# Optimization experiments

Measured on AMD Instinct MI355X. Metric: run time of the kernel, lower is better.

Reference implementation:

```python
import jax, jax.numpy as jnp
import numpy as np

B = 4194304
RAD2DEG = 180.0 / np.pi


def setup_inputs() -> dict:
    key = jax.random.key(0)
    k1, k2, k3 = jax.random.split(key, 3)
    label = jax.random.normal(k1, (B, 3, 2), dtype=jnp.float32)
    est_label = jax.random.normal(k2, (B, 6), dtype=jnp.float32)
    mix_way = jax.random.randint(k3, (B,), 0, 2, dtype=jnp.int32)  # 0='single', 1=mixed
    return {"label": label, "est_label": est_label, "mix_way": mix_way}


def reference(label, est_label, mix_way):
    # --- permutation-invariant MSE loss ---
    e1, e2 = est_label[:, :3], est_label[:, 3:]            # [B,3] each
    l1, l2 = label[:, :, 0], label[:, :, 1]                 # [B,3] each
    mse = lambda a, b: jnp.mean((a - b) ** 2, axis=-1)      # per-batch mean over 3 comps
    loss_perm1 = mse(e1, l1) + mse(e2, l2)                  # [B]
    loss_perm2 = mse(e2, l1) + mse(e1, l2)                  # [B]
    mixed_loss = jnp.minimum(loss_perm1, loss_perm2)        # [B]
    # 'single' branch in the original uses the FULL (unindexed) tensors -> same scalar each time
    single_loss = jnp.mean((est_label[:, :3] - label[:, :, 0]) ** 2)
    per_batch = jnp.where(mix_way == 0, single_loss, mixed_loss)
    label_loss = jnp.mean(per_batch)

    # --- azimuth MAE with angle wrap-around and best pairing ---
    lab_az1 = jnp.arctan2(label[:, 1, 0], label[:, 0, 0]) * RAD2DEG
    lab_az2 = jnp.arctan2(label[:, 1, 1], label[:, 0, 1]) * RAD2DEG
    est_az1 = jnp.arctan2(est_label[:, 1], est_label[:, 0]) * RAD2DEG
    est_az2 = jnp.arctan2(est_label[:, 4], est_label[:, 3]) * RAD2DEG

    def wrap(e):
        e = jnp.abs(e)
        return jnp.where(e > 180.0, 360.0 - e, e)

    e11 = wrap(lab_az1 - est_az1)
    e22 = wrap(lab_az2 - est_az2)
    e12 = wrap(lab_az1 - est_az2)
    e21 = wrap(lab_az2 - est_az1)

    use_direct = (e11 + e22) < (e12 + e21)
    mae1 = jnp.mean(jnp.where(use_direct, e11, e12))
    mae2 = jnp.mean(jnp.where(use_direct, e22, e21))

    return (label_loss, mae1, mae2)
```

## Files before the change

### kernel.cpp

```cpp
#include <hip/hip_runtime.h>
#include <math.h>

#define RAD2DEG 57.29577951308232f

constexpr int S1_BLOCKS = 2048;
constexpr int S1_TPB    = 256;
constexpr int CHUNK     = 256;
constexpr int CH_F      = CHUNK * 12;
constexpr int CH_V4     = CHUNK * 3;

typedef __attribute__((address_space(1))) const unsigned int gu32;
typedef __attribute__((address_space(3))) unsigned int       lu32;

__device__ __forceinline__ void g2lds16(const float4* g, float* lds) {
    __builtin_amdgcn_global_load_lds((gu32*)g, (lu32*)lds, 16, 0, 0);
}

__device__ __forceinline__ float angdist_deg(float ax, float ay,
                                             float bx, float by) {
    float dot = ax * bx + ay * by;
    float cr  = fabsf(ay * bx - ax * by);
    float ad  = fabsf(dot);
    float mn  = fminf(cr, ad);
    float mx  = fmaxf(cr, ad);
    float t   = mn * __builtin_amdgcn_rcpf(fmaxf(mx, 1e-37f));
    float s   = t * t;
    float p = fmaf(s, -0.01172120f, 0.05265332f);
    p = fmaf(s, p, -0.11643287f);
    p = fmaf(s, p,  0.19354346f);
    p = fmaf(s, p, -0.33262347f);
    p = fmaf(s, p,  0.99997726f);
    float a = t * p;
    a = (cr > ad)    ? (1.57079632679489662f - a) : a;
    a = (dot < 0.0f) ? (3.14159265358979323f - a) : a;
    return a * RAD2DEG;
}

__device__ __forceinline__ void per_row(
    float l1x, float l2x, float l1y, float l2y, float l1z, float l2z,
    float e1x, float e1y, float e1z, float e2x, float e2y, float e2z,
    int mw,
    float& sS, float& sM, float& sC0, float& sM1, float& sM2)
{
    float dx, dy, dz;
    dx = e1x - l1x; dy = e1y - l1y; dz = e1z - l1z;
    float d11 = dx*dx + dy*dy + dz*dz;
    dx = e2x - l2x; dy = e2y - l2y; dz = e2z - l2z;
    float d22 = dx*dx + dy*dy + dz*dz;
    dx = e2x - l1x; dy = e2y - l1y; dz = e2z - l1z;
    float d21 = dx*dx + dy*dy + dz*dz;
    dx = e1x - l2x; dy = e1y - l2y; dz = e1z - l2z;
    float d12 = dx*dx + dy*dy + dz*dz;

    sS += d11;

    float mixed = fminf(d11 + d22, d21 + d12) * (1.0f / 3.0f);
    float m = (mw != 0) ? 1.0f : 0.0f;
    sM  += m * mixed;
    sC0 += 1.0f - m;

    float e11 = angdist_deg(l1x, l1y, e1x, e1y);
    float e22 = angdist_deg(l2x, l2y, e2x, e2y);
    float e12 = angdist_deg(l1x, l1y, e2x, e2y);
    float e21 = angdist_deg(l2x, l2y, e1x, e1y);

    bool ud = (e11 + e22) < (e12 + e21);
    sM1 += ud ? e11 : e12;
    sM2 += ud ? e22 : e21;
}

__global__ __launch_bounds__(S1_TPB) void stage1_kernel(
    const float* __restrict__ label,
    const float* __restrict__ est,
    const int*   __restrict__ mix,
    float* __restrict__ partials,
    int P)
{
    __shared__ float labS[CH_F];
    __shared__ float estS[CH_F];

    const int tid  = threadIdx.x;
    const int wid  = tid >> 6;
    const int lane = tid & 63;

    const float4* lab4 = (const float4*)label;
    const float4* est4 = (const float4*)est;
    const int2*   mix2 = (const int2*)mix;

    float sS = 0.f, sM = 0.f, sC0 = 0.f, sM1 = 0.f, sM2 = 0.f;

    const int nchunks = P / CHUNK;
    for (int c = blockIdx.x; c < nchunks; c += gridDim.x) {
        const int vbase = c * CH_V4;
        #pragma unroll
        for (int j = 0; j < 3; ++j) {
            const int vi = j * 256 + wid * 64;
            g2lds16(lab4 + vbase + vi + lane, labS + vi * 4);
            g2lds16(est4 + vbase + vi + lane, estS + vi * 4);
        }
        int2 mw = mix2[c * CHUNK + tid];
        __syncthreads();

        const float4* Lv = (const float4*)(labS + tid * 12);
        const float4* Ev = (const float4*)(estS + tid * 12);
        float4 L0 = Lv[0], L1 = Lv[1], L2 = Lv[2];
        float4 E0 = Ev[0], E1 = Ev[1], E2 = Ev[2];

        per_row(L0.x, L0.y, L0.z, L0.w, L1.x, L1.y,
                E0.x, E0.y, E0.z, E0.w, E1.x, E1.y,
                mw.x, sS, sM, sC0, sM1, sM2);
        per_row(L1.z, L1.w, L2.x, L2.y, L2.z, L2.w,
                E1.z, E1.w, E2.x, E2.y, E2.z, E2.w,
                mw.y, sS, sM, sC0, sM1, sM2);
        __syncthreads();
    }

    for (int p = nchunks * CHUNK + blockIdx.x * S1_TPB + tid; p < P;
         p += gridDim.x * S1_TPB) {
        const float4* lv = (const float4*)(label + (size_t)p * 12);
        const float4* ev = (const float4*)(est   + (size_t)p * 12);
        float4 L0 = lv[0], L1 = lv[1], L2 = lv[2];
        float4 E0 = ev[0], E1 = ev[1], E2 = ev[2];
        int2 mw = mix2[p];
        per_row(L0.x, L0.y, L0.z, L0.w, L1.x, L1.y,
                E0.x, E0.y, E0.z, E0.w, E1.x, E1.y,
                mw.x, sS, sM, sC0, sM1, sM2);
        per_row(L1.z, L1.w, L2.x, L2.y, L2.z, L2.w,
                E1.z, E1.w, E2.x, E2.y, E2.z, E2.w,
                mw.y, sS, sM, sC0, sM1, sM2);
    }

    for (int off = 32; off > 0; off >>= 1) {
        sS  += __shfl_down(sS,  off, 64);
        sM  += __shfl_down(sM,  off, 64);
        sC0 += __shfl_down(sC0, off, 64);
        sM1 += __shfl_down(sM1, off, 64);
        sM2 += __shfl_down(sM2, off, 64);
    }

    __shared__ float red[S1_TPB / 64][5];
    if (lane == 0) {
        red[wid][0] = sS; red[wid][1] = sM; red[wid][2] = sC0;
        red[wid][3] = sM1; red[wid][4] = sM2;
    }
    __syncthreads();
    if (tid == 0) {
        float r0 = 0.f, r1 = 0.f, r2 = 0.f, r3 = 0.f, r4 = 0.f;
        #pragma unroll
        for (int w = 0; w < S1_TPB / 64; ++w) {
            r0 += red[w][0]; r1 += red[w][1]; r2 += red[w][2];
            r3 += red[w][3]; r4 += red[w][4];
        }
        float* out = partials + (size_t)blockIdx.x * 5;
        out[0] = r0; out[1] = r1; out[2] = r2; out[3] = r3; out[4] = r4;
    }
}

__global__ __launch_bounds__(256) void stage2_kernel(
    const float* __restrict__ partials,
    float* __restrict__ out,
    int nblocks,
    long long Btot)
{
    const int tid = threadIdx.x;
    double aS = 0, aM = 0, aC0 = 0, aM1 = 0, aM2 = 0;
    for (int r = tid; r < nblocks; r += 256) {
        const float* row = partials + (size_t)r * 5;
        aS += row[0]; aM += row[1]; aC0 += row[2]; aM1 += row[3]; aM2 += row[4];
    }
    for (int off = 32; off > 0; off >>= 1) {
        aS  += __shfl_down(aS,  off, 64);
        aM  += __shfl_down(aM,  off, 64);
        aC0 += __shfl_down(aC0, off, 64);
        aM1 += __shfl_down(aM1, off, 64);
        aM2 += __shfl_down(aM2, off, 64);
    }
    __shared__ double red[4][5];
    const int wid = tid >> 6, lane = tid & 63;
    if (lane == 0) {
        red[wid][0] = aS; red[wid][1] = aM; red[wid][2] = aC0;
        red[wid][3] = aM1; red[wid][4] = aM2;
    }
    __syncthreads();
    if (tid == 0) {
        double S = 0, M = 0, C0 = 0, M1 = 0, M2 = 0;
        #pragma unroll
        for (int w = 0; w < 4; ++w) {
            S += red[w][0]; M += red[w][1]; C0 += red[w][2];
            M1 += red[w][3]; M2 += red[w][4];
        }
        const double Bd = (double)Btot;
        const double single_loss = S / (3.0 * Bd);
        out[0] = (float)((C0 * single_loss + M) / Bd);
        out[1] = (float)(M1 / Bd);
        out[2] = (float)(M2 / Bd);
    }
}

extern "C" void kernel_launch(void* const* d_in, const int* in_sizes, int n_in,
                              void* d_out, int out_size, void* d_ws, size_t ws_size,
                              hipStream_t stream) {
    const float* label = (const float*)d_in[0];
    const float* est   = (const float*)d_in[1];
    const int*   mix   = (const int*)d_in[2];
    float* out = (float*)d_out;
    float* partials = (float*)d_ws;

    const long long B = (long long)in_sizes[2];
    const int P = (int)(B / 2);

    stage1_kernel<<<S1_BLOCKS, S1_TPB, 0, stream>>>(label, est, mix, partials, P);
    stage2_kernel<<<1, 256, 0, stream>>>(partials, out, S1_BLOCKS, B);
}
```

Before: 231.5 us.

## Replace LDS-staged chunk loads with direct strided float4 loads, two pairs per iteration

Drops the global_load_lds staging through shared memory and the two barriers per chunk. Each thread now loads its own 48-byte rows straight from global memory and handles two row-pairs per iteration to keep more loads in flight. The cost is uncoalesced strided float4 accesses, since adjacent lanes read addresses 48 bytes apart, and higher register pressure.

```diff
diff --git a/kernel.cpp b/kernel.cpp
--- a/kernel.cpp
+++ b/kernel.cpp
@@ -5,16 +5,6 @@
 
 constexpr int S1_BLOCKS = 2048;
 constexpr int S1_TPB    = 256;
-constexpr int CHUNK     = 256;
-constexpr int CH_F      = CHUNK * 12;
-constexpr int CH_V4     = CHUNK * 3;
-
-typedef __attribute__((address_space(1))) const unsigned int gu32;
-typedef __attribute__((address_space(3))) unsigned int       lu32;
-
-__device__ __forceinline__ void g2lds16(const float4* g, float* lds) {
-    __builtin_amdgcn_global_load_lds((gu32*)g, (lu32*)lds, 16, 0, 0);
-}
 
 __device__ __forceinline__ float angdist_deg(float ax, float ay,
                                              float bx, float by) {
@@ -76,12 +66,11 @@
     float* __restrict__ partials,
     int P)
 {
-    __shared__ float labS[CH_F];
-    __shared__ float estS[CH_F];
-
-    const int tid  = threadIdx.x;
-    const int wid  = tid >> 6;
-    const int lane = tid & 63;
+    const int tid   = threadIdx.x;
+    const int wid   = tid >> 6;
+    const int lane  = tid & 63;
+    const int gsize = gridDim.x * S1_TPB;
+    const int g     = blockIdx.x * S1_TPB + tid;
 
     const float4* lab4 = (const float4*)label;
     const float4* est4 = (const float4*)est;
@@ -89,38 +78,39 @@
 
     float sS = 0.f, sM = 0.f, sC0 = 0.f, sM1 = 0.f, sM2 = 0.f;
 
-    const int nchunks = P / CHUNK;
-    for (int c = blockIdx.x; c < nchunks; c += gridDim.x) {
-        const int vbase = c * CH_V4;
-        #pragma unroll
-        for (int j = 0; j < 3; ++j) {
-            const int vi = j * 256 + wid * 64;
-            g2lds16(lab4 + vbase + vi + lane, labS + vi * 4);
-            g2lds16(est4 + vbase + vi + lane, estS + vi * 4);
-        }
-        int2 mw = mix2[c * CHUNK + tid];
-        __syncthreads();
-
-        const float4* Lv = (const float4*)(labS + tid * 12);
-        const float4* Ev = (const float4*)(estS + tid * 12);
-        float4 L0 = Lv[0], L1 = Lv[1], L2 = Lv[2];
-        float4 E0 = Ev[0], E1 = Ev[1], E2 = Ev[2];
-
-        per_row(L0.x, L0.y, L0.z, L0.w, L1.x, L1.y,
-                E0.x, E0.y, E0.z, E0.w, E1.x, E1.y,
-                mw.x, sS, sM, sC0, sM1, sM2);
-        per_row(L1.z, L1.w, L2.x, L2.y, L2.z, L2.w,
-                E1.z, E1.w, E2.x, E2.y, E2.z, E2.w,
-                mw.y, sS, sM, sC0, sM1, sM2);
-        __syncthreads();
-    }
-
-    for (int p = nchunks * CHUNK + blockIdx.x * S1_TPB + tid; p < P;
-         p += gridDim.x * S1_TPB) {
-        const float4* lv = (const float4*)(label + (size_t)p * 12);
-        const float4* ev = (const float4*)(est   + (size_t)p * 12);
-        float4 L0 = lv[0], L1 = lv[1], L2 = lv[2];
-        float4 E0 = ev[0], E1 = ev[1], E2 = ev[2];
+    int p = g;
+    for (; p + gsize < P; p += 2 * gsize) {
+        const int q = p + gsize;
+        const float4* lp = lab4 + (size_t)p * 3;
+        const float4* ep = est4 + (size_t)p * 3;
+        const float4* lq = lab4 + (size_t)q * 3;
+        const float4* eq = est4 + (size_t)q * 3;
+
+        float4 La0 = lp[0], La1 = lp[1], La2 = lp[2];
+        float4 Ea0 = ep[0], Ea1 = ep[1], Ea2 = ep[2];
+        float4 Lb0 = lq[0], Lb1 = lq[1], Lb2 = lq[2];
+        float4 Eb0 = eq[0], Eb1 = eq[1], Eb2 = eq[2];
+        int2 ma = mix2[p];
+        int2 mb = mix2[q];
+
+        per_row(La0.x, La0.y, La0.z, La0.w, La1.x, La1.y,
+                Ea0.x, Ea0.y, Ea0.z, Ea0.w, Ea1.x, Ea1.y,
+                ma.x, sS, sM, sC0, sM1, sM2);
+        per_row(La1.z, La1.w, La2.x, La2.y, La2.z, La2.w,
+                Ea1.z, Ea1.w, Ea2.x, Ea2.y, Ea2.z, Ea2.w,
+                ma.y, sS, sM, sC0, sM1, sM2);
+        per_row(Lb0.x, Lb0.y, Lb0.z, Lb0.w, Lb1.x, Lb1.y,
+                Eb0.x, Eb0.y, Eb0.z, Eb0.w, Eb1.x, Eb1.y,
+                mb.x, sS, sM, sC0, sM1, sM2);
+        per_row(Lb1.z, Lb1.w, Lb2.x, Lb2.y, Lb2.z, Lb2.w,
+                Eb1.z, Eb1.w, Eb2.x, Eb2.y, Eb2.z, Eb2.w,
+                mb.y, sS, sM, sC0, sM1, sM2);
+    }
+    if (p < P) {
+        const float4* lp = lab4 + (size_t)p * 3;
+        const float4* ep = est4 + (size_t)p * 3;
+        float4 L0 = lp[0], L1 = lp[1], L2 = lp[2];
+        float4 E0 = ep[0], E1 = ep[1], E2 = ep[2];
         int2 mw = mix2[p];
         per_row(L0.x, L0.y, L0.z, L0.w, L1.x, L1.y,
                 E0.x, E0.y, E0.z, E0.w, E1.x, E1.y,
```

New measurement: 228.3 us. About the same (-1.4%).

## Double-buffer LDS staging per wave and drop block barriers in stage1

Applied to the files above, without the earlier changes.

Stage1 now double-buffers the global-to-LDS async copies. The next chunk's loads are issued before the current chunk is computed, and the code waits with explicit vmcnt counts instead of __syncthreads. The per-wave load mapping changes so each wave stages exactly the rows its own threads consume, which makes block-wide barriers unnecessary. The grid shrinks from 2048 to 768 blocks so each block loops over more chunks, at the cost of doubled LDS use and fewer resident blocks to hide latency.

```diff
diff --git a/kernel.cpp b/kernel.cpp
--- a/kernel.cpp
+++ b/kernel.cpp
@@ -3,16 +3,19 @@
 
 #define RAD2DEG 57.29577951308232f
 
-constexpr int S1_BLOCKS = 2048;
+constexpr int S1_BLOCKS = 768;
 constexpr int S1_TPB    = 256;
 constexpr int CHUNK     = 256;
 constexpr int CH_F      = CHUNK * 12;
 constexpr int CH_V4     = CHUNK * 3;
 
+typedef float f32x4 __attribute__((ext_vector_type(4)));
+typedef int   i32x2 __attribute__((ext_vector_type(2)));
+
 typedef __attribute__((address_space(1))) const unsigned int gu32;
 typedef __attribute__((address_space(3))) unsigned int       lu32;
 
-__device__ __forceinline__ void g2lds16(const float4* g, float* lds) {
+__device__ __forceinline__ void g2lds16(const f32x4* g, float* lds) {
     __builtin_amdgcn_global_load_lds((gu32*)g, (lu32*)lds, 16, 0, 0);
 }
 
@@ -69,6 +72,20 @@
     sM2 += ud ? e22 : e21;
 }
 
+__device__ __forceinline__ void per_pair(
+    const f32x4& L0, const f32x4& L1, const f32x4& L2,
+    const f32x4& E0, const f32x4& E1, const f32x4& E2,
+    const i32x2& mw,
+    float& sS, float& sM, float& sC0, float& sM1, float& sM2)
+{
+    per_row(L0.x, L0.y, L0.z, L0.w, L1.x, L1.y,
+            E0.x, E0.y, E0.z, E0.w, E1.x, E1.y,
+            mw.x, sS, sM, sC0, sM1, sM2);
+    per_row(L1.z, L1.w, L2.x, L2.y, L2.z, L2.w,
+            E1.z, E1.w, E2.x, E2.y, E2.z, E2.w,
+            mw.y, sS, sM, sC0, sM1, sM2);
+}
+
 __global__ __launch_bounds__(S1_TPB) void stage1_kernel(
     const float* __restrict__ label,
     const float* __restrict__ est,
@@ -76,58 +93,69 @@
     float* __restrict__ partials,
     int P)
 {
-    __shared__ float labS[CH_F];
-    __shared__ float estS[CH_F];
+    __shared__ float labS[2][CH_F];
+    __shared__ float estS[2][CH_F];
 
     const int tid  = threadIdx.x;
     const int wid  = tid >> 6;
     const int lane = tid & 63;
 
-    const float4* lab4 = (const float4*)label;
-    const float4* est4 = (const float4*)est;
-    const int2*   mix2 = (const int2*)mix;
+    const f32x4* lab4 = (const f32x4*)label;
+    const f32x4* est4 = (const f32x4*)est;
+    const i32x2* mix2 = (const i32x2*)mix;
 
     float sS = 0.f, sM = 0.f, sC0 = 0.f, sM1 = 0.f, sM2 = 0.f;
 
+#define STAGE(c_, buf_) do {                                            \
+        const int vbase_ = (c_) * CH_V4;                                \
+        _Pragma("unroll")                                               \
+        for (int j = 0; j < 3; ++j) {                                   \
+            const int vi = wid * 192 + j * 64;   \
+            g2lds16(lab4 + vbase_ + vi + lane, &labS[buf_][vi * 4]);    \
+            g2lds16(est4 + vbase_ + vi + lane, &estS[buf_][vi * 4]);    \
+        }                                                               \
+    } while (0)
+
     const int nchunks = P / CHUNK;
-    for (int c = blockIdx.x; c < nchunks; c += gridDim.x) {
-        const int vbase = c * CH_V4;
-        #pragma unroll
-        for (int j = 0; j < 3; ++j) {
-            const int vi = j * 256 + wid * 64;
-            g2lds16(lab4 + vbase + vi + lane, labS + vi * 4);
-            g2lds16(est4 + vbase + vi + lane, estS + vi * 4);
+    int c = blockIdx.x;
+    if (c < nchunks) {
+        int buf = 0;
+        STAGE(c, 0);
+        while (true) {
+            const int cn = c + gridDim.x;
+            const bool have_next = (cn < nchunks);
+
+            i32x2 mw = mix2[c * CHUNK + tid];
+            __builtin_amdgcn_sched_barrier(0);
+            if (have_next) {
+                STAGE(cn, buf ^ 1);
+                asm volatile("s_waitcnt vmcnt(6)" ::: "memory");
+            } else {
+                asm volatile("s_waitcnt vmcnt(0)" ::: "memory");
+            }
+            __builtin_amdgcn_sched_barrier(0);
+
+            const f32x4* Lv = (const f32x4*)(&labS[buf][tid * 12]);
+            const f32x4* Ev = (const f32x4*)(&estS[buf][tid * 12]);
+            f32x4 L0 = Lv[0], L1 = Lv[1], L2 = Lv[2];
+            f32x4 E0 = Ev[0], E1 = Ev[1], E2 = Ev[2];
+            per_pair(L0, L1, L2, E0, E1, E2, mw, sS, sM, sC0, sM1, sM2);
+
+            if (!have_next) break;
+            c = cn;
+            buf ^= 1;
         }
-        int2 mw = mix2[c * CHUNK + tid];
-        __syncthreads();
-
-        const float4* Lv = (const float4*)(labS + tid * 12);
-        const float4* Ev = (const float4*)(estS + tid * 12);
-        float4 L0 = Lv[0], L1 = Lv[1], L2 = Lv[2];
-        float4 E0 = Ev[0], E1 = Ev[1], E2 = Ev[2];
-
-        per_row(L0.x, L0.y, L0.z, L0.w, L1.x, L1.y,
-                E0.x, E0.y, E0.z, E0.w, E1.x, E1.y,
-                mw.x, sS, sM, sC0, sM1, sM2);
-        per_row(L1.z, L1.w, L2.x, L2.y, L2.z, L2.w,
-                E1.z, E1.w, E2.x, E2.y, E2.z, E2.w,
-                mw.y, sS, sM, sC0, sM1, sM2);
-        __syncthreads();
-    }
+    }
+#undef STAGE
 
     for (int p = nchunks * CHUNK + blockIdx.x * S1_TPB + tid; p < P;
          p += gridDim.x * S1_TPB) {
-        const float4* lv = (const float4*)(label + (size_t)p * 12);
-        const float4* ev = (const float4*)(est   + (size_t)p * 12);
-        float4 L0 = lv[0], L1 = lv[1], L2 = lv[2];
-        float4 E0 = ev[0], E1 = ev[1], E2 = ev[2];
-        int2 mw = mix2[p];
-        per_row(L0.x, L0.y, L0.z, L0.w, L1.x, L1.y,
-                E0.x, E0.y, E0.z, E0.w, E1.x, E1.y,
-                mw.x, sS, sM, sC0, sM1, sM2);
-        per_row(L1.z, L1.w, L2.x, L2.y, L2.z, L2.w,
-                E1.z, E1.w, E2.x, E2.y, E2.z, E2.w,
-                mw.y, sS, sM, sC0, sM1, sM2);
+        const f32x4* lp = (const f32x4*)(label + (size_t)p * 12);
+        const f32x4* ep = (const f32x4*)(est   + (size_t)p * 12);
+        f32x4 L0 = lp[0], L1 = lp[1], L2 = lp[2];
+        f32x4 E0 = ep[0], E1 = ep[1], E2 = ep[2];
+        i32x2 mw = mix2[p];
+        per_pair(L0, L1, L2, E0, E1, E2, mw, sS, sM, sC0, sM1, sM2);
     }
 
     for (int off = 32; off > 0; off >>= 1) {
```

Measured after the change: 229.0 us. Within noise of the previous version (-1.1%).
